# Optimization experiments

Measured on AMD Instinct MI355X. Metric: run time of the kernel, lower is better.

## Reference

```python
import jax, jax.numpy as jnp
import numpy as np

D_MODEL = 4096
D_FIBER = 16
D_CONTROL = 64
EMA_MOMENTUM = 0.9


def setup_inputs() -> dict:
    key = jax.random.key(0)
    k_h, k_f, k_w1, k_w2 = jax.random.split(key, 4)
    B, S = 4, 2048
    hidden = jax.random.normal(k_h, (B, S, D_MODEL), dtype=jnp.float32)
    # torch nn.Linear stores weight as [out, in]; fiber_proj init: normal std=0.02
    W_fiber = jax.random.normal(k_f, (D_FIBER, D_MODEL), dtype=jnp.float32) * 0.02
    # predictor[0]: Linear(d_model+d_fiber, d_control) with default torch init (uniform)
    fan_in1 = D_MODEL + D_FIBER
    bound1 = 1.0 / np.sqrt(fan_in1)
    W1 = jax.random.uniform(k_w1, (D_CONTROL, fan_in1), dtype=jnp.float32, minval=-bound1, maxval=bound1)
    b1 = jnp.zeros((D_CONTROL,), dtype=jnp.float32)
    # predictor[-2]: Linear(d_control, 1), weight normal std=0.01, bias zero
    W2 = jax.random.normal(k_w2, (1, D_CONTROL), dtype=jnp.float32) * 0.01
    b2 = jnp.zeros((1,), dtype=jnp.float32)
    lam = jnp.asarray(1.0, dtype=jnp.float32)
    return {"hidden": hidden, "W_fiber": W_fiber, "W1": W1, "b1": b1, "W2": W2, "b2": b2, "lam": lam}


def _causal_ema(delta_h, alpha):
    # h_t = alpha*h_{t-1} + (1-alpha)*d_t, h_{-1} = 0. delta_h: [B,S]
    B = delta_h.shape[0]
    def step(h_prev, d_t):
        h_t = alpha * h_prev + (1.0 - alpha) * d_t
        return h_t, h_t
    _, hs = jax.lax.scan(step, jnp.zeros((B,), delta_h.dtype), jnp.swapaxes(delta_h, 0, 1))
    return jnp.swapaxes(hs, 0, 1)  # [B,S]


def reference(hidden, W_fiber, W1, b1, W2, b2, lam):
    h = hidden.astype(jnp.float32)                      # [B,S,D]
    fiber = jnp.einsum('bsd,fd->bsf', h, W_fiber)       # [B,S,16]
    combined = jnp.concatenate([h, fiber], axis=-1)     # [B,S,D+16]
    z = jax.nn.gelu(jnp.einsum('bsc,kc->bsk', combined, W1) + b1, approximate=False)
    delta_h = jax.nn.softplus(jnp.einsum('bsk,ok->bso', z, W2) + b2)[..., 0]  # [B,S]
    field = _causal_ema(delta_h, EMA_MOMENTUM)          # [B,S]
    gate = jax.nn.sigmoid(-lam * field)
    return gate.astype(hidden.dtype), field.astype(hidden.dtype), delta_h.mean()
```

## Files before the change

kernel.cpp:

```cpp
#include <hip/hip_runtime.h>
#include <hip/hip_bf16.h>

#define D_MODEL 4096
#define NTOK    8192
#define SEQ     2048

typedef short bf16x8 __attribute__((ext_vector_type(8)));
typedef float f32x4  __attribute__((ext_vector_type(4)));

__device__ __forceinline__ short f2bf(float x) {
  __hip_bfloat16 h = __float2bfloat16(x);
  return *reinterpret_cast<short*>(&h);
}
__device__ __forceinline__ float bfs2f(unsigned short u) {
  unsigned int x = ((unsigned int)u) << 16;
  float f;
  __builtin_memcpy(&f, &x, 4);
  return f;
}
__device__ __forceinline__ float bf2f(const void* p, size_t i) {
  return bfs2f(((const unsigned short*)p)[i]);
}

__device__ __forceinline__ int sniff_wave(const unsigned short* p, int n) {
  int lane = threadIdx.x & 63;
  int S = n / 2 < 64 ? n / 2 : 64;
  bool act = lane < S;
  unsigned short ve = 0, vo = 0;
  if (act) { ve = p[2 * lane]; vo = p[2 * lane + 1]; }
  int ee = (ve >> 7) & 0xFF, eo = (vo >> 7) & 0xFF;
  bool ve_band   = (ve == 0) || (ve == 0x8000) || (ee >= 96 && ee <= 141);
  bool vo_bandnz = (vo != 0) && (vo != 0x8000) && (eo >= 96 && eo <= 141);
  int zp = __popcll(__ballot(act && ve == 0 && vo == 0));
  int ob = __popcll(__ballot(act && ve == 0 && vo_bandnz));
  int eb = __popcll(__ballot(act && ve_band));
  if (zp == S) return 1;
  if (4 * ob >= 3 * S) return 0;
  if (4 * eb >= 3 * S) return 1;
  return 0;
}

__device__ __forceinline__ float decode_lam(const void* lamp) {
  unsigned short l0 = *(const unsigned short*)lamp;
  int le = (l0 >> 7) & 0xFF;
  if (l0 != 0 && l0 != 0x8000 && le >= 96 && le <= 141)
    return bfs2f(l0);
  return *(const float*)lamp;
}
__device__ __forceinline__ float decode_b2(const void* p) {
  unsigned short c0 = *(const unsigned short*)p;
  int ce = (c0 >> 7) & 0xFF;
  if (c0 == 0) return 0.0f;
  if (c0 != 0x8000 && ce >= 96 && ce <= 141)
    return bfs2f(c0);
  return *(const float*)p;
}

__global__ __launch_bounds__(256) void fold_w1(const void* __restrict__ W1v,
                                               const void* __restrict__ Wfv,
                                               short* __restrict__ W1eff) {
  int n = blockIdx.x;
  int fw1 = sniff_wave((const unsigned short*)W1v, 64 * 4112);
  int fwf = sniff_wave((const unsigned short*)Wfv, 16 * D_MODEL);
  __shared__ float w1b[16];
  if (threadIdx.x < 16) {
    size_t idx = (size_t)n * 4112 + 4096 + threadIdx.x;
    w1b[threadIdx.x] = fw1 ? bf2f(W1v, idx) : ((const float*)W1v)[idx];
  }
  __syncthreads();
  for (int it = 0; it < 4; ++it) {
    int k0 = it * 1024 + threadIdx.x * 4;
    size_t idx = (size_t)n * 4112 + k0;
    float v0, v1, v2, v3;
    if (fw1) {
      ushort4 u = *(const ushort4*)((const unsigned short*)W1v + idx);
      v0 = bfs2f(u.x); v1 = bfs2f(u.y); v2 = bfs2f(u.z); v3 = bfs2f(u.w);
    } else {
      float4 f = *(const float4*)((const float*)W1v + idx);
      v0 = f.x; v1 = f.y; v2 = f.z; v3 = f.w;
    }
#pragma unroll
    for (int f = 0; f < 16; ++f) {
      size_t wi = (size_t)f * D_MODEL + k0;
      float w0, w1_, w2_, w3_;
      if (fwf) {
        ushort4 u = *(const ushort4*)((const unsigned short*)Wfv + wi);
        w0 = bfs2f(u.x); w1_ = bfs2f(u.y); w2_ = bfs2f(u.z); w3_ = bfs2f(u.w);
      } else {
        float4 fv = *(const float4*)((const float*)Wfv + wi);
        w0 = fv.x; w1_ = fv.y; w2_ = fv.z; w3_ = fv.w;
      }
      float s = w1b[f];
      v0 += s * w0; v1 += s * w1_; v2 += s * w2_; v3 += s * w3_;
    }
    ushort4 o;
    o.x = (unsigned short)f2bf(v0); o.y = (unsigned short)f2bf(v1);
    o.z = (unsigned short)f2bf(v2); o.w = (unsigned short)f2bf(v3);
    *(ushort4*)(W1eff + (size_t)n * D_MODEL + k0) = o;
  }
}

__device__ __forceinline__ void stage_chunk(short* Bs, const short* __restrict__ B_,
                                            int c, int w, int lane) {
#pragma unroll
  for (int i = 0; i < 8; ++i) {
    int n = w + i * 8;
    bf16x8 v = *(const bf16x8*)(B_ + (size_t)n * D_MODEL + c * 512 + lane * 8);
    *(bf16x8*)(Bs + lane * 512 + ((n ^ (lane & 7)) * 8)) = v;
  }
}

__global__ __launch_bounds__(512, 4) void gemm_fused(const void* __restrict__ hid,
                                                     const short* __restrict__ B_,
                                                     const void* __restrict__ b1,
                                                     const void* __restrict__ w2,
                                                     const void* __restrict__ b2,
                                                     float* __restrict__ delta) {
  int t = blockIdx.x;
  int w = threadIdx.x >> 6, lane = threadIdx.x & 63;
  int wc = w & 3, kc = w >> 2;
  int m = lane & 15, kg = lane >> 4;

  __shared__ short Bs[64 * 512];
  __shared__ float red[16][68];

  int fhid = sniff_wave((const unsigned short*)hid, NTOK * D_MODEL);

  f32x4 acc = {0.f, 0.f, 0.f, 0.f};
  size_t abase = (size_t)(t * 16 + m) * D_MODEL + kc * 256 + kg * 8;

  if (fhid) {
    const short* Ap = (const short*)hid + abase;
    bf16x8 areg[2][8];
#pragma unroll
    for (int s = 0; s < 8; ++s) areg[0][s] = *(const bf16x8*)(Ap + s * 32);
#pragma unroll
    for (int c = 0; c < 8; ++c) {
      __syncthreads();
      if (c < 7) {
#pragma unroll
        for (int s = 0; s < 8; ++s)
          areg[(c + 1) & 1][s] = *(const bf16x8*)(Ap + (c + 1) * 512 + s * 32);
      }
      stage_chunk(Bs, B_, c, w, lane);
      __syncthreads();
#pragma unroll
      for (int s = 0; s < 8; ++s) {
        int kb16 = kc * 32 + s * 4 + kg;
        bf16x8 b = *(const bf16x8*)(Bs + kb16 * 512 + (((wc * 16 + m) ^ (kb16 & 7)) * 8));
        acc = __builtin_amdgcn_mfma_f32_16x16x32_bf16(areg[c & 1][s], b, acc, 0, 0, 0);
      }
    }
  } else {
    const float* Ap = (const float*)hid + abase;
    for (int c = 0; c < 8; ++c) {
      __syncthreads();
      stage_chunk(Bs, B_, c, w, lane);
      __syncthreads();
#pragma unroll
      for (int s = 0; s < 8; ++s) {
        float4 lo = *(const float4*)(Ap + c * 512 + s * 32);
        float4 hi = *(const float4*)(Ap + c * 512 + s * 32 + 4);
        bf16x8 a;
        a[0] = f2bf(lo.x); a[1] = f2bf(lo.y); a[2] = f2bf(lo.z); a[3] = f2bf(lo.w);
        a[4] = f2bf(hi.x); a[5] = f2bf(hi.y); a[6] = f2bf(hi.z); a[7] = f2bf(hi.w);
        int kb16 = kc * 32 + s * 4 + kg;
        bf16x8 b = *(const bf16x8*)(Bs + kb16 * 512 + (((wc * 16 + m) ^ (kb16 & 7)) * 8));
        acc = __builtin_amdgcn_mfma_f32_16x16x32_bf16(a, b, acc, 0, 0, 0);
      }
    }
  }

  if (kc == 1) {
#pragma unroll
    for (int r = 0; r < 4; ++r) red[kg * 4 + r][wc * 16 + m] = acc[r];
  }
  __syncthreads();
  float b2v = 0.f;
  if (kc == 0) {
    int fb1 = sniff_wave((const unsigned short*)b1, 64);
    int fw2 = sniff_wave((const unsigned short*)w2, 64);
    b2v = decode_b2(b2);
    int col = wc * 16 + m;
    float b1v = fb1 ? bf2f(b1, col) : ((const float*)b1)[col];
    float w2v = fw2 ? bf2f(w2, col) : ((const float*)w2)[col];
#pragma unroll
    for (int r = 0; r < 4; ++r) {
      int tok = kg * 4 + r;
      float s = acc[r] + red[tok][col] + b1v;
      float g = 0.5f * s * (1.0f + erff(s * 0.70710678118654752f));
      red[tok][col] = g * w2v;
    }
  }
  __syncthreads();
  if (threadIdx.x < 16) {
    float y = 0.f;
#pragma unroll
    for (int cc = 0; cc < 64; ++cc) y += red[threadIdx.x][cc];
    float x = y + b2v;
    float d = (x > 20.0f) ? x : log1pf(expf(x));
    delta[t * 16 + threadIdx.x] = d;
  }
}

__global__ __launch_bounds__(256) void ema_out(const float* __restrict__ delta,
                                               const void* __restrict__ lamp,
                                               float* __restrict__ out) {
  int b    = threadIdx.x >> 6;
  int lane = threadIdx.x & 63;
  const float alpha = 0.9f;
  float d[32];
  const float* dp = delta + b * SEQ + lane * 32;
  float beta = 0.f, lsum = 0.f;
#pragma unroll
  for (int i = 0; i < 32; ++i) {
    d[i] = dp[i];
    lsum += d[i];
    beta = alpha * beta + 0.1f * d[i];
  }
  float accA = 0.03433683820292512f;
  float accB = beta;
  for (int off = 1; off < 64; off <<= 1) {
    float uA = __shfl_up(accA, off, 64);
    float uB = __shfl_up(accB, off, 64);
    if (lane >= off) {
      accB = accB + accA * uB;
      accA = accA * uA;
    }
  }
  float prev = __shfl_up(accB, 1, 64);
  float h = (lane == 0) ? 0.f : prev;
  float lam = decode_lam(lamp);
#pragma unroll
  for (int i = 0; i < 32; ++i) {
    h = alpha * h + 0.1f * d[i];
    float gate = 1.0f / (1.0f + expf(lam * h));
    out[b * SEQ + lane * 32 + i]        = gate;
    out[NTOK + b * SEQ + lane * 32 + i] = h;
  }
#pragma unroll
  for (int off = 32; off >= 1; off >>= 1) lsum += __shfl_xor(lsum, off, 64);
  __shared__ float bs[4];
  if (lane == 0) bs[b] = lsum;
  __syncthreads();
  if (threadIdx.x == 0)
    out[2 * NTOK] = (bs[0] + bs[1] + bs[2] + bs[3]) * (1.0f / 8192.0f);
}

extern "C" void kernel_launch(void* const* d_in, const int* in_sizes, int n_in,
                              void* d_out, int out_size, void* d_ws, size_t ws_size,
                              hipStream_t stream) {
  const void* hidden = d_in[0];
  const void* Wf     = d_in[1];
  const void* W1     = d_in[2];
  const void* b1     = d_in[3];
  const void* W2     = d_in[4];
  const void* b2     = d_in[5];
  const void* lam    = d_in[6];
  float* out = (float*)d_out;

  char* ws = (char*)d_ws;
  short* W1eff = (short*)ws;
  float* delta = (float*)(ws + (size_t)64 * D_MODEL * 2);

  fold_w1<<<64, 256, 0, stream>>>(W1, Wf, W1eff);
  gemm_fused<<<512, 512, 0, stream>>>(hidden, W1eff, b1, W2, b2, delta);
  ema_out<<<1, 256, 0, stream>>>(delta, lam, out);
}
```

Before: 248.0 us.

## Stream weight fragments directly from global memory, split K across all waves

Replaces the LDS-staged B tile and its per-chunk barriers with direct global loads of weight fragments into registers, double-buffered per step. Each of the 8 waves now owns a 512-wide K slice and computes all 64 output columns with four accumulators, followed by an 8-way LDS reduction. The epilogue is reworked so 256 threads handle GELU and the W2 dot product, using a shuffle reduction. This removes the syncthreads and LDS traffic on the main loop, at the cost of more redundant L2 reads of the small weight matrix and a larger reduction buffer.

```diff
diff --git a/kernel.cpp b/kernel.cpp
--- a/kernel.cpp
+++ b/kernel.cpp
@@ -100,106 +100,104 @@
   }
 }
 
-__device__ __forceinline__ void stage_chunk(short* Bs, const short* __restrict__ B_,
-                                            int c, int w, int lane) {
-#pragma unroll
-  for (int i = 0; i < 8; ++i) {
-    int n = w + i * 8;
-    bf16x8 v = *(const bf16x8*)(B_ + (size_t)n * D_MODEL + c * 512 + lane * 8);
-    *(bf16x8*)(Bs + lane * 512 + ((n ^ (lane & 7)) * 8)) = v;
-  }
-}
-
-__global__ __launch_bounds__(512, 4) void gemm_fused(const void* __restrict__ hid,
-                                                     const short* __restrict__ B_,
-                                                     const void* __restrict__ b1,
-                                                     const void* __restrict__ w2,
-                                                     const void* __restrict__ b2,
-                                                     float* __restrict__ delta) {
+__global__ __launch_bounds__(512, 4) void gemm_stream(const void* __restrict__ hid,
+                                                      const short* __restrict__ B_,
+                                                      const void* __restrict__ b1,
+                                                      const void* __restrict__ w2,
+                                                      const void* __restrict__ b2,
+                                                      float* __restrict__ delta) {
   int t = blockIdx.x;
   int w = threadIdx.x >> 6, lane = threadIdx.x & 63;
-  int wc = w & 3, kc = w >> 2;
   int m = lane & 15, kg = lane >> 4;
 
-  __shared__ short Bs[64 * 512];
-  __shared__ float red[16][68];
+  __shared__ float red[8][16][68];
 
   int fhid = sniff_wave((const unsigned short*)hid, NTOK * D_MODEL);
 
-  f32x4 acc = {0.f, 0.f, 0.f, 0.f};
-  size_t abase = (size_t)(t * 16 + m) * D_MODEL + kc * 256 + kg * 8;
+  f32x4 acc0 = {0.f, 0.f, 0.f, 0.f};
+  f32x4 acc1 = acc0, acc2 = acc0, acc3 = acc0;
+
+  size_t abase = (size_t)(t * 16 + m) * D_MODEL + w * 512 + kg * 8;
+  const short* Bp = B_ + (size_t)m * D_MODEL + w * 512 + kg * 8;
 
   if (fhid) {
     const short* Ap = (const short*)hid + abase;
-    bf16x8 areg[2][8];
-#pragma unroll
-    for (int s = 0; s < 8; ++s) areg[0][s] = *(const bf16x8*)(Ap + s * 32);
-#pragma unroll
-    for (int c = 0; c < 8; ++c) {
-      __syncthreads();
-      if (c < 7) {
-#pragma unroll
-        for (int s = 0; s < 8; ++s)
-          areg[(c + 1) & 1][s] = *(const bf16x8*)(Ap + (c + 1) * 512 + s * 32);
+    bf16x8 ar[2], br[2][4];
+#pragma unroll
+    for (int p = 0; p < 2; ++p) {
+      ar[p] = *(const bf16x8*)(Ap + p * 32);
+#pragma unroll
+      for (int nc = 0; nc < 4; ++nc)
+        br[p][nc] = *(const bf16x8*)(Bp + (size_t)nc * 16 * D_MODEL + p * 32);
+    }
+#pragma unroll
+    for (int s = 0; s < 16; ++s) {
+      int cur = s & 1;
+      bf16x8 a  = ar[cur];
+      bf16x8 f0 = br[cur][0], f1 = br[cur][1], f2 = br[cur][2], f3 = br[cur][3];
+      if (s + 2 < 16) {
+        ar[cur] = *(const bf16x8*)(Ap + (s + 2) * 32);
+#pragma unroll
+        for (int nc = 0; nc < 4; ++nc)
+          br[cur][nc] = *(const bf16x8*)(Bp + (size_t)nc * 16 * D_MODEL + (s + 2) * 32);
       }
-      stage_chunk(Bs, B_, c, w, lane);
-      __syncthreads();
-#pragma unroll
-      for (int s = 0; s < 8; ++s) {
-        int kb16 = kc * 32 + s * 4 + kg;
-        bf16x8 b = *(const bf16x8*)(Bs + kb16 * 512 + (((wc * 16 + m) ^ (kb16 & 7)) * 8));
-        acc = __builtin_amdgcn_mfma_f32_16x16x32_bf16(areg[c & 1][s], b, acc, 0, 0, 0);
-      }
+      acc0 = __builtin_amdgcn_mfma_f32_16x16x32_bf16(a, f0, acc0, 0, 0, 0);
+      acc1 = __builtin_amdgcn_mfma_f32_16x16x32_bf16(a, f1, acc1, 0, 0, 0);
+      acc2 = __builtin_amdgcn_mfma_f32_16x16x32_bf16(a, f2, acc2, 0, 0, 0);
+      acc3 = __builtin_amdgcn_mfma_f32_16x16x32_bf16(a, f3, acc3, 0, 0, 0);
     }
   } else {
     const float* Ap = (const float*)hid + abase;
-    for (int c = 0; c < 8; ++c) {
-      __syncthreads();
-      stage_chunk(Bs, B_, c, w, lane);
-      __syncthreads();
-#pragma unroll
-      for (int s = 0; s < 8; ++s) {
-        float4 lo = *(const float4*)(Ap + c * 512 + s * 32);
-        float4 hi = *(const float4*)(Ap + c * 512 + s * 32 + 4);
-        bf16x8 a;
-        a[0] = f2bf(lo.x); a[1] = f2bf(lo.y); a[2] = f2bf(lo.z); a[3] = f2bf(lo.w);
-        a[4] = f2bf(hi.x); a[5] = f2bf(hi.y); a[6] = f2bf(hi.z); a[7] = f2bf(hi.w);
-        int kb16 = kc * 32 + s * 4 + kg;
-        bf16x8 b = *(const bf16x8*)(Bs + kb16 * 512 + (((wc * 16 + m) ^ (kb16 & 7)) * 8));
-        acc = __builtin_amdgcn_mfma_f32_16x16x32_bf16(a, b, acc, 0, 0, 0);
+    for (int s = 0; s < 16; ++s) {
+      float4 lo = *(const float4*)(Ap + s * 32);
+      float4 hi = *(const float4*)(Ap + s * 32 + 4);
+      bf16x8 a;
+      a[0] = f2bf(lo.x); a[1] = f2bf(lo.y); a[2] = f2bf(lo.z); a[3] = f2bf(lo.w);
+      a[4] = f2bf(hi.x); a[5] = f2bf(hi.y); a[6] = f2bf(hi.z); a[7] = f2bf(hi.w);
+#pragma unroll
+      for (int nc = 0; nc < 4; ++nc) {
+        bf16x8 bb = *(const bf16x8*)(Bp + (size_t)nc * 16 * D_MODEL + s * 32);
+        if (nc == 0) acc0 = __builtin_amdgcn_mfma_f32_16x16x32_bf16(a, bb, acc0, 0, 0, 0);
+        if (nc == 1) acc1 = __builtin_amdgcn_mfma_f32_16x16x32_bf16(a, bb, acc1, 0, 0, 0);
+        if (nc == 2) acc2 = __builtin_amdgcn_mfma_f32_16x16x32_bf16(a, bb, acc2, 0, 0, 0);
+        if (nc == 3) acc3 = __builtin_amdgcn_mfma_f32_16x16x32_bf16(a, bb, acc3, 0, 0, 0);
       }
     }
   }
 
-  if (kc == 1) {
-#pragma unroll
-    for (int r = 0; r < 4; ++r) red[kg * 4 + r][wc * 16 + m] = acc[r];
+#pragma unroll
+  for (int r = 0; r < 4; ++r) {
+    int tok = kg * 4 + r;
+    red[w][tok][m +  0] = acc0[r];
+    red[w][tok][m + 16] = acc1[r];
+    red[w][tok][m + 32] = acc2[r];
+    red[w][tok][m + 48] = acc3[r];
   }
   __syncthreads();
-  float b2v = 0.f;
-  if (kc == 0) {
+
+  if (threadIdx.x < 256) {
+    int tok = threadIdx.x >> 4;
+    int cid = threadIdx.x & 15;
     int fb1 = sniff_wave((const unsigned short*)b1, 64);
     int fw2 = sniff_wave((const unsigned short*)w2, 64);
-    b2v = decode_b2(b2);
-    int col = wc * 16 + m;
-    float b1v = fb1 ? bf2f(b1, col) : ((const float*)b1)[col];
-    float w2v = fw2 ? bf2f(w2, col) : ((const float*)w2)[col];
-#pragma unroll
-    for (int r = 0; r < 4; ++r) {
-      int tok = kg * 4 + r;
-      float s = acc[r] + red[tok][col] + b1v;
+    float y = 0.f;
+#pragma unroll
+    for (int j = 0; j < 4; ++j) {
+      int col = cid + 16 * j;
+      float s = 0.f;
+#pragma unroll
+      for (int q = 0; q < 8; ++q) s += red[q][tok][col];
+      s += fb1 ? bf2f(b1, col) : ((const float*)b1)[col];
       float g = 0.5f * s * (1.0f + erff(s * 0.70710678118654752f));
-      red[tok][col] = g * w2v;
-    }
-  }
-  __syncthreads();
-  if (threadIdx.x < 16) {
-    float y = 0.f;
-#pragma unroll
-    for (int cc = 0; cc < 64; ++cc) y += red[threadIdx.x][cc];
-    float x = y + b2v;
-    float d = (x > 20.0f) ? x : log1pf(expf(x));
-    delta[t * 16 + threadIdx.x] = d;
+      y += g * (fw2 ? bf2f(w2, col) : ((const float*)w2)[col]);
+    }
+#pragma unroll
+    for (int off = 1; off <= 8; off <<= 1) y += __shfl_xor(y, off, 64);
+    if (cid == 0) {
+      float x = y + decode_b2(b2);
+      float d = (x > 20.0f) ? x : log1pf(expf(x));
+      delta[t * 16 + tok] = d;
+    }
   }
 }
 
@@ -264,6 +262,6 @@
   float* delta = (float*)(ws + (size_t)64 * D_MODEL * 2);
 
   fold_w1<<<64, 256, 0, stream>>>(W1, Wf, W1eff);
-  gemm_fused<<<512, 512, 0, stream>>>(hidden, W1eff, b1, W2, b2, delta);
+  gemm_stream<<<512, 512, 0, stream>>>(hidden, W1eff, b1, W2, b2, delta);
   ema_out<<<1, 256, 0, stream>>>(delta, lam, out);
 }
```

Result: faster. 237.2 us (-4.4%).
